# Kernel tuning notes

Measured on AMD Instinct MI355X. Metric: run time of the kernel, lower is better.

## Reference

```python
import jax, jax.numpy as jnp
import numpy as np

B, Q, D = 4, 1024, 1024
N, DH = 16, 64  # n_head, d_head
SCALE = 1.0 / DH ** 0.5
LN_EPS = 1e-5


def setup_inputs() -> dict:
    key = jax.random.key(0)
    ks = jax.random.split(key, 10)
    return {
        "w": jax.random.normal(ks[0], (B, Q, D), jnp.float32),
        "r_emb": jax.random.normal(ks[1], (Q, N, DH), jnp.float32),
        "r_w_bias": jax.random.normal(ks[2], (N, DH), jnp.float32),
        "r_bias": jax.random.normal(ks[3], (Q, N), jnp.float32),
        # projection weights stored [in, out]; torch Linear init std = 1/sqrt(d_head)
        "Wq": jax.random.normal(ks[4], (D, N * DH), jnp.float32) * SCALE,
        "Wk": jax.random.normal(ks[5], (D, N * DH), jnp.float32) * SCALE,
        "Wv": jax.random.normal(ks[6], (D, N * DH), jnp.float32) * SCALE,
        "Wo": jax.random.normal(ks[7], (N * DH, D), jnp.float32) * SCALE,
        "ln_gamma": jnp.ones((D,), jnp.float32),
        "ln_beta": jnp.zeros((D,), jnp.float32),
    }


def _rel_shift(x):
    # x: [b, i, j, n]; pad a zero column at the end of j then drop j=0
    # equivalent to shifting left by one along j with a trailing zero.
    return jnp.concatenate([x[:, :, 1:, :], jnp.zeros_like(x[:, :, :1, :])], axis=2)


def reference(w, r_emb, r_w_bias, r_bias, Wq, Wk, Wv, Wo, ln_gamma, ln_beta):
    b, qlen, d = w.shape
    klen = qlen  # mems=None
    n, dh = r_w_bias.shape

    q_h = (w @ Wq).reshape(b, qlen, n, dh)
    k_h = (w @ Wk).reshape(b, klen, n, dh)
    v_h = (w @ Wv).reshape(b, klen, n, dh)

    rw_q = q_h + r_w_bias[None, None]                      # [b,q,n,dh]
    AC = jnp.einsum('bind,bjnd->bijn', rw_q, k_h)          # [b,q,k,n]
    B_ = jnp.einsum('bind,jnd->bijn', q_h, r_emb)          # [b,q,k,n]
    BD = _rel_shift(B_ + r_bias[None, None])               # [b,q,k,n]

    attn_score = (AC + BD) * SCALE
    attn_prob = jax.nn.softmax(attn_score, axis=2)
    attn_vec = jnp.einsum('bijn,bjnd->bind', attn_prob, v_h)
    attn_out = attn_vec.reshape(b, qlen, n * dh) @ Wo

    out = w + attn_out  # residual (post-lnorm path)
    mu = jnp.mean(out, axis=-1, keepdims=True)
    var = jnp.var(out, axis=-1, keepdims=True)
    return (out - mu) / jnp.sqrt(var + LN_EPS) * ln_gamma + ln_beta
```

## Files before the change

### kernel.cpp

```cpp
#include <hip/hip_runtime.h>
#include <hip/hip_bf16.h>

using f16 = _Float16;
typedef _Float16 f16x8 __attribute__((ext_vector_type(8)));
typedef _Float16 f16x4 __attribute__((ext_vector_type(4)));
typedef float f32x4 __attribute__((ext_vector_type(4)));

#define AS1 __attribute__((address_space(1)))
#define AS3 __attribute__((address_space(3)))

constexpr int Bc = 4, Qc = 1024, Dc = 1024, Nh = 16, DHc = 64;
constexpr int BQ = Bc * Qc;
constexpr int NHEAD = Bc * Nh;
constexpr float ATT_SCALE = 0.125f;
constexpr float LOG2E = 1.44269504088896f;

struct Ptr4 { const float* p[4]; };
__global__ __launch_bounds__(256) void k_prep(
    const float* __restrict__ w_in, f16* __restrict__ wh,
    Ptr4 srcs, f16* __restrict__ WT,
    const float* __restrict__ remb, f16* __restrict__ Ke)
{
    const int bid = blockIdx.x, tid = threadIdx.x;
    if (bid < 2048) {
        long i8 = ((long)bid * 256 + tid) * 8;
        float4 a = *(const float4*)&w_in[i8];
        float4 b = *(const float4*)&w_in[i8 + 4];
        f16x8 o = { (f16)a.x, (f16)a.y, (f16)a.z, (f16)a.w,
                    (f16)b.x, (f16)b.y, (f16)b.z, (f16)b.w };
        *(f16x8*)&wh[i8] = o;
    } else if (bid < 6144) {
        __shared__ f16 tile[32][33];
        int idx = bid - 2048;
        int z = idx >> 10, rem = idx & 1023;
        int r0 = (rem >> 5) * 32, c0 = (rem & 31) * 32;
        const float* src = srcs.p[z];
        f16* d = WT + (long)z * Dc * Dc;
        int tx = tid & 31, ty = tid >> 5;
#pragma unroll
        for (int dy = 0; dy < 32; dy += 8) {
            int r = r0 + ty + dy, c = c0 + tx;
            tile[ty + dy][tx] = (f16)src[(long)r * Dc + c];
        }
        __syncthreads();
#pragma unroll
        for (int dy = 0; dy < 32; dy += 8) {
            int c = c0 + ty + dy, r = r0 + tx;
            d[(long)c * Dc + r] = tile[tx][ty + dy];
        }
    } else {
        long gid = (long)(bid - 6144) * 256 + tid;
        int d8 = (int)(gid & 7) * 8;
        int j = (int)((gid >> 3) & 1023);
        int h = (int)(gid >> 13);
        int n = h & 15;
        f16x8 kv;
        if (j < 1023) {
            const float* rp = &remb[((long)(j + 1) * 16 + n) * 64 + d8];
            float4 r0 = *(const float4*)rp, r1 = *(const float4*)(rp + 4);
            kv[0] = (f16)r0.x; kv[1] = (f16)r0.y; kv[2] = (f16)r0.z; kv[3] = (f16)r0.w;
            kv[4] = (f16)r1.x; kv[5] = (f16)r1.y; kv[6] = (f16)r1.z; kv[7] = (f16)r1.w;
        } else {
            kv = f16x8{};
        }
        *(f16x8*)&Ke[(((long)h << 10) + j) * 64 + d8] = kv;
    }
}

__global__ __launch_bounds__(256) void k_fold(
    f16* __restrict__ kh, const f16* __restrict__ Ke,
    const float* __restrict__ rwb, const float* __restrict__ rbias,
    float* __restrict__ ckrb)
{
    long gid = (long)blockIdx.x * 256 + threadIdx.x;
    int t8 = (int)(gid & 7);
    long seg = gid >> 3;
    int n = (int)(seg & 15);
    long gm = seg >> 4;
    int b = (int)(gm >> 10), j = (int)(gm & 1023);

    f16* kp = &kh[gm * 1024 + n * 64 + t8 * 8];
    f16x8 kv = *(f16x8*)kp;
    f16x8 ke = *(const f16x8*)&Ke[(((long)(b * 16 + n) << 10) + j) * 64 + t8 * 8];

    float dot = 0.0f;
    f16x8 ko;
#pragma unroll
    for (int e = 0; e < 8; ++e) {
        float kf = (float)kv[e];
        dot += kf * rwb[n * 64 + t8 * 8 + e];
        ko[e] = (f16)(kf + (float)ke[e]);
    }
    *(f16x8*)kp = ko;

    dot += __shfl_xor(dot, 1);
    dot += __shfl_xor(dot, 2);
    dot += __shfl_xor(dot, 4);
    if (t8 == 0) {
        float rbv = (j < 1023) ? rbias[(j + 1) * 16 + n] : 0.0f;
        ckrb[(((long)(b * 16 + n)) << 10) + j] = (dot + rbv) * (ATT_SCALE * LOG2E);
    }
}

template <int BM, int BN, int BK, int WROWS, int WCOLS, int EPI>
__global__ __launch_bounds__(256) void k_gemm_nt(
    const f16* __restrict__ A, const f16* __restrict__ Bt, void* __restrict__ Cv,
    f16* __restrict__ qtp, f16* __restrict__ ktp, f16* __restrict__ vtp,
    int lda, int ldb, int ldc, int K)
{
    static_assert(BK == 64, "geometry below assumes BK=64");
    constexpr int TM = BM / (WROWS * 16);
    constexpr int TN = BN / (WCOLS * 16);
    __shared__ __align__(16) f16 sA[BM * 64];
    __shared__ __align__(16) f16 sB[BN * 64];

    const int tid = threadIdx.x;
    const int lane = tid & 63, wave = tid >> 6;
    const int wm = wave / WCOLS, wn = wave % WCOLS;

    const int nwg = gridDim.x * gridDim.y;
    const int flat = blockIdx.y * gridDim.x + blockIdx.x;
    const int cpx = nwg >> 3;
    const int swz = (flat & 7) * cpx + (flat >> 3);
    const int bx = swz % gridDim.x, by = swz / gridDim.x;
    const int m0 = by * BM, n0 = bx * BN;

    f32x4 acc[TM][TN] = {};

    const int lrow = lane & 15;
    const int quad = lane >> 4;
    const int srow = lane >> 3;
    const int scol = ((lane & 7) ^ (srow & 7)) * 8;

    for (int k0 = 0; k0 < K; k0 += 64) {
        __syncthreads();
        constexpr int CHA = BM / 8;
#pragma unroll
        for (int ch = 0; ch < CHA / 4; ++ch) {
            int cc = ch * 4 + wave;
            __builtin_amdgcn_global_load_lds(
                (const AS1 void*)(const void*)&A[(long)(m0 + cc * 8 + srow) * lda + k0 + scol],
                (AS3 void*)(void*)&sA[cc * 512], 16, 0, 0);
        }
        constexpr int CHB = BN / 8;
#pragma unroll
        for (int ch = 0; ch < CHB / 4; ++ch) {
            int cc = ch * 4 + wave;
            __builtin_amdgcn_global_load_lds(
                (const AS1 void*)(const void*)&Bt[(long)(n0 + cc * 8 + srow) * ldb + k0 + scol],
                (AS3 void*)(void*)&sB[cc * 512], 16, 0, 0);
        }
        __syncthreads();

#pragma unroll
        for (int kk = 0; kk < 2; ++kk) {
            const int kcb = kk * 4 + quad;
            f16x8 af[TM], bfr[TN];
#pragma unroll
            for (int mi = 0; mi < TM; ++mi) {
                int R = wm * TM * 16 + mi * 16 + lrow;
                af[mi] = *(const f16x8*)&sA[R * 64 + ((kcb ^ (lrow & 7)) * 8)];
            }
#pragma unroll
            for (int ni = 0; ni < TN; ++ni) {
                int R = wn * TN * 16 + ni * 16 + lrow;
                bfr[ni] = *(const f16x8*)&sB[R * 64 + ((kcb ^ (lrow & 7)) * 8)];
            }
#pragma unroll
            for (int mi = 0; mi < TM; ++mi)
#pragma unroll
                for (int ni = 0; ni < TN; ++ni)
                    acc[mi][ni] = __builtin_amdgcn_mfma_f32_16x16x32_f16(af[mi], bfr[ni], acc[mi][ni], 0, 0, 0);
        }
    }

    const int crow = (lane >> 4) * 4;
    const int ccol = lane & 15;
#pragma unroll
    for (int mi = 0; mi < TM; ++mi)
#pragma unroll
        for (int ni = 0; ni < TN; ++ni)
#pragma unroll
            for (int r = 0; r < 4; ++r) {
                int gm = m0 + wm * TM * 16 + mi * 16 + crow + r;
                int gn = n0 + wn * TN * 16 + ni * 16 + ccol;
                float val = acc[mi][ni][r];
                if constexpr (EPI == 0) {
                    ((f16*)Cv)[(long)gm * ldc + gn] = (f16)val;
                } else {
                    int seg = n0 >> 10;
                    int col = gn & 1023;
                    if (seg == 0) {
                        qtp[(long)gm * 1024 + col] = (f16)val;
                    } else if (seg == 1) {
                        ktp[(long)gm * 1024 + col] = (f16)val;
                    } else {
                        int b = gm >> 10, i = gm & 1023;
                        vtp[(((long)(b << 10) + col) << 10) + i] = (f16)val;
                    }
                }
            }
}

__global__ __launch_bounds__(512, 4) void k_flash(
    const f16* __restrict__ qh, const f16* __restrict__ kh,
    const f16* __restrict__ vT, const float* __restrict__ ckrb,
    f16* __restrict__ avp)
{
    __shared__ __align__(16) f16 sKa[2][128 * 64];
    __shared__ __align__(16) f16 sVa[2][64 * 128];
    __shared__ float sRB[2][128];

    const int tid = threadIdx.x, lane = tid & 63, wave = tid >> 6;
    const int bid = blockIdx.x;
    const int h = (((bid >> 3) & 7) << 3) | (bid & 7);
    const int i0 = (bid >> 6) * 128;
    const int b = h >> 4, n = h & 15;

    const int lrow = lane & 15;
    const int quad = lane >> 4;

    const int lr3 = lane >> 3;
    const int swcK = (lane & 7) ^ (lr3 & 7);
    const f16* srcK = kh + ((long)(b * Qc) + 16 * wave + lr3) * 1024 + n * 64 + swcK * 8;

    const int lv4 = lane >> 4;
    const int c16 = lane & 15;
    const int d0 = 8 * wave + lv4;
    const int swcV0 = (c16 & 8) | ((c16 & 7) ^ (d0 & 7));
    const int swcV1 = (c16 & 8) | ((c16 & 7) ^ ((d0 + 4) & 7));
    const f16* srcVb = vT + (long)h * DHc * Qc;

    const f16 qsc = (f16)0.125f;
    f16x8 aq[2];
    {
        long rix = (long)(b * Qc + i0 + wave * 16 + lrow) * 1024 + n * 64;
        aq[0] = *(const f16x8*)&qh[rix + quad * 8] * qsc;
        aq[1] = *(const f16x8*)&qh[rix + 32 + quad * 8] * qsc;
    }

    auto stage = [&](int buf, int j0) {
        __builtin_amdgcn_global_load_lds((const AS1 void*)(srcK + (long)j0 * 1024),
                                         (AS3 void*)&sKa[buf][wave * 1024], 16, 0, 0);
        __builtin_amdgcn_global_load_lds((const AS1 void*)(srcK + (long)(j0 + 8) * 1024),
                                         (AS3 void*)&sKa[buf][wave * 1024 + 512], 16, 0, 0);
        __builtin_amdgcn_global_load_lds((const AS1 void*)(srcVb + (long)d0 * Qc + j0 + swcV0 * 8),
                                         (AS3 void*)&sVa[buf][wave * 1024], 16, 0, 0);
        __builtin_amdgcn_global_load_lds((const AS1 void*)(srcVb + (long)(d0 + 4) * Qc + j0 + swcV1 * 8),
                                         (AS3 void*)&sVa[buf][wave * 1024 + 512], 16, 0, 0);
    };

    float m_i = -1e30f, l_i = 0.0f;
    f32x4 o_acc[4] = {};

    {
        float rbv = 0.0f;
        if (tid < 128) rbv = ckrb[((long)h << 10) + tid];
        stage(0, 0);
        if (tid < 128) sRB[0][tid] = rbv;
    }
    __syncthreads();

    for (int jt = 0; jt < 8; ++jt) {
        const int cur = jt & 1;

        float rbn = 0.0f;
        if (jt < 7) {
            const int j0n = (jt + 1) * 128;
            stage(cur ^ 1, j0n);
            if (tid < 128) rbn = ckrb[((long)h << 10) + j0n + tid];
        }

        const f16* Ka = &sKa[cur][0];
        const f16* Va = &sVa[cur][0];
        const int rsw = lrow & 7;

        f32x4 s_acc[8] = {};
#pragma unroll
        for (int ni = 0; ni < 8; ++ni) {
            int rb_ = (ni * 16 + lrow) * 64;
            f16x8 a0 = *(const f16x8*)&Ka[rb_ + ((0 + quad) ^ rsw) * 8];
            f16x8 a1 = *(const f16x8*)&Ka[rb_ + ((4 + quad) ^ rsw) * 8];
            s_acc[ni] = __builtin_amdgcn_mfma_f32_16x16x32_f16(a0, aq[0], s_acc[ni], 0, 0, 0);
            s_acc[ni] = __builtin_amdgcn_mfma_f32_16x16x32_f16(a1, aq[1], s_acc[ni], 0, 0, 0);
        }

        f16x4 pf[8];
        float mx = -1e30f, sm = 0.0f;
#pragma unroll
        for (int ni = 0; ni < 8; ++ni) {
            f32x4 rb4 = *(const f32x4*)&sRB[cur][ni * 16 + quad * 4];
            f16x4 pvv;
#pragma unroll
            for (int r = 0; r < 4; ++r) {
                float v = fmaf(s_acc[ni][r], LOG2E, rb4[r]);
                s_acc[ni][r] = v;
                mx = fmaxf(mx, v);
                float e = __builtin_amdgcn_exp2f(v - m_i);
                sm += e;
                pvv[r] = (f16)e;
            }
            pf[ni] = pvv;
        }
        if (!__all(mx - m_i <= 8.0f)) {
            float wmx = fmaxf(mx, __shfl_xor(mx, 16));
            wmx = fmaxf(wmx, __shfl_xor(wmx, 32));
            float mn = fmaxf(m_i, wmx);
            float alpha = __builtin_amdgcn_exp2f(m_i - mn);
            sm = 0.0f;
#pragma unroll
            for (int ni = 0; ni < 8; ++ni) {
                f16x4 pvv;
#pragma unroll
                for (int r = 0; r < 4; ++r) {
                    float e = __builtin_amdgcn_exp2f(s_acc[ni][r] - mn);
                    sm += e;
                    pvv[r] = (f16)e;
                }
                pf[ni] = pvv;
            }
            l_i *= alpha;
#pragma unroll
            for (int r = 0; r < 4; ++r) {
                float al = __shfl(alpha, quad * 4 + r);
#pragma unroll
                for (int dt = 0; dt < 4; ++dt) o_acc[dt][r] *= al;
            }
            m_i = mn;
        }
        l_i += sm;

#pragma unroll
        for (int nj = 0; nj < 8; ++nj) {
            int c = 2 * nj + (quad >> 1);
            int coff = ((c & 8) | ((c & 7) ^ rsw)) * 8 + (quad & 1) * 4;
#pragma unroll
            for (int dt = 0; dt < 4; ++dt) {
                f16x4 bv = *(const f16x4*)&Va[(dt * 16 + lrow) * 128 + coff];
                o_acc[dt] = __builtin_amdgcn_mfma_f32_16x16x16f16(pf[nj], bv, o_acc[dt], 0, 0, 0);
            }
        }

        if (jt < 7) {
            if (tid < 128) sRB[cur ^ 1][tid] = rbn;
            __syncthreads();
        }
    }

    l_i += __shfl_xor(l_i, 16);
    l_i += __shfl_xor(l_i, 32);
    {
        float linv = 1.0f / l_i;
#pragma unroll
        for (int r = 0; r < 4; ++r) {
            float li = __shfl(linv, quad * 4 + r);
            int i = i0 + wave * 16 + quad * 4 + r;
#pragma unroll
            for (int dt = 0; dt < 4; ++dt) {
                int d = dt * 16 + lrow;
                avp[((long)(b * Qc + i) << 10) + n * 64 + d] = (f16)(o_acc[dt][r] * li);
            }
        }
    }
}

__global__ __launch_bounds__(256) void k_res_ln(const float* __restrict__ w, const f16* __restrict__ ao,
                                                const float* __restrict__ gamma, const float* __restrict__ beta,
                                                float* __restrict__ out) {
    const long base = (long)blockIdx.x * 1024;
    const int tid = threadIdx.x;
    float4 wv = *(const float4*)&w[base + tid * 4];
    f16x4 av = *(const f16x4*)&ao[base + tid * 4];
    float x[4] = { wv.x + (float)av[0], wv.y + (float)av[1],
                   wv.z + (float)av[2], wv.w + (float)av[3] };
    float s = x[0] + x[1] + x[2] + x[3];
    float s2 = x[0] * x[0] + x[1] * x[1] + x[2] * x[2] + x[3] * x[3];
#pragma unroll
    for (int off = 32; off; off >>= 1) { s += __shfl_down(s, off); s2 += __shfl_down(s2, off); }
    __shared__ float rs[4], rs2[4];
    if ((tid & 63) == 0) { rs[tid >> 6] = s; rs2[tid >> 6] = s2; }
    __syncthreads();
    s = rs[0] + rs[1] + rs[2] + rs[3];
    s2 = rs2[0] + rs2[1] + rs2[2] + rs2[3];
    float mu = s * (1.0f / 1024.0f);
    float var = s2 * (1.0f / 1024.0f) - mu * mu;
    float inv = rsqrtf(var + 1e-5f);
    float4 gv = *(const float4*)&gamma[tid * 4];
    float4 bv = *(const float4*)&beta[tid * 4];
    float4 o;
    o.x = (x[0] - mu) * inv * gv.x + bv.x;
    o.y = (x[1] - mu) * inv * gv.y + bv.y;
    o.z = (x[2] - mu) * inv * gv.z + bv.z;
    o.w = (x[3] - mu) * inv * gv.w + bv.w;
    *(float4*)&out[base + tid * 4] = o;
}

extern "C" void kernel_launch(void* const* d_in, const int* in_sizes, int n_in,
                              void* d_out, int out_size, void* d_ws, size_t ws_size,
                              hipStream_t stream) {
    const float* w_in   = (const float*)d_in[0];
    const float* r_emb  = (const float*)d_in[1];
    const float* r_wb   = (const float*)d_in[2];
    const float* r_bias = (const float*)d_in[3];
    const float* Wq     = (const float*)d_in[4];
    const float* Wk     = (const float*)d_in[5];
    const float* Wv     = (const float*)d_in[6];
    const float* Wo     = (const float*)d_in[7];
    const float* ln_g   = (const float*)d_in[8];
    const float* ln_b   = (const float*)d_in[9];
    float* out = (float*)d_out;

    char* p = (char*)d_ws;
    auto alloc = [&](size_t bytes) { char* r = p; p += (bytes + 255) & ~(size_t)255; return r; };
    f16* wh = (f16*)alloc((size_t)BQ * Dc * 2);
    f16* WT = (f16*)alloc((size_t)4 * Dc * Dc * 2);
    f16* qh = (f16*)alloc((size_t)BQ * Dc * 2);
    f16* kh = (f16*)alloc((size_t)BQ * Dc * 2);
    f16* Ke = (f16*)alloc((size_t)NHEAD * Qc * DHc * 2);
    f16* vT = (f16*)alloc((size_t)BQ * Dc * 2);
    float* ckrb = (float*)alloc((size_t)NHEAD * Qc * 4);
    f16* WoT = WT + (size_t)3 * Dc * Dc;
    f16* avp = wh;
    f16* ao  = Ke;

    Ptr4 srcs{{Wq, Wk, Wv, Wo}};
    k_prep<<<8192, 256, 0, stream>>>(w_in, wh, srcs, WT, r_emb, Ke);

    k_gemm_nt<128, 128, 64, 2, 2, 5><<<dim3(3 * Dc / 128, BQ / 128), 256, 0, stream>>>(
        wh, WT, nullptr, qh, kh, vT, Dc, Dc, 0, Dc);

    k_fold<<<2048, 256, 0, stream>>>(kh, Ke, r_wb, r_bias, ckrb);

    k_flash<<<512, 512, 0, stream>>>(qh, kh, vT, ckrb, avp);

    k_gemm_nt<64, 128, 64, 2, 2, 0><<<dim3(Dc / 128, BQ / 64), 256, 0, stream>>>(
        avp, WoT, ao, nullptr, nullptr, nullptr, Dc, Dc, Dc, Dc);

    k_res_ln<<<BQ, 256, 0, stream>>>(w_in, ao, ln_g, ln_b, out);
}
```

Before: 200.4 us.

## Triple-buffer GEMM LDS staging with BK=32 and async prefetch two tiles ahead

Restructures the NT GEMM main loop from a single-buffered BK=64 tile, with two barriers per iteration, into a three-stage ring of BK=32 LDS buffers. Direct global-to-LDS loads for tile kt+2 are issued before computing tile kt, and explicit vmcnt waits plus one barrier per step replace the old sync pattern. This is meant to hide global load latency behind MFMA work in both the QKV and output projections. In exchange there are more loop iterations with fewer MFMAs each, a new LDS swizzle for 32-wide rows, and manual vmcnt counting that must match the number of issued loads.

Result: slower. 205.4 us (+2.5%).

```diff
diff --git a/kernel.cpp b/kernel.cpp
--- a/kernel.cpp
+++ b/kernel.cpp
@@ -102,17 +102,17 @@
     }
 }
 
-template <int BM, int BN, int BK, int WROWS, int WCOLS, int EPI>
+template <int BM, int BN, int WROWS, int WCOLS, int EPI>
 __global__ __launch_bounds__(256) void k_gemm_nt(
     const f16* __restrict__ A, const f16* __restrict__ Bt, void* __restrict__ Cv,
     f16* __restrict__ qtp, f16* __restrict__ ktp, f16* __restrict__ vtp,
     int lda, int ldb, int ldc, int K)
 {
-    static_assert(BK == 64, "geometry below assumes BK=64");
     constexpr int TM = BM / (WROWS * 16);
     constexpr int TN = BN / (WCOLS * 16);
-    __shared__ __align__(16) f16 sA[BM * 64];
-    __shared__ __align__(16) f16 sB[BN * 64];
+    constexpr int LPS = BM / 64 + BN / 64;
+    __shared__ __align__(16) f16 sA[3][BM * 32];
+    __shared__ __align__(16) f16 sB[3][BN * 32];
 
     const int tid = threadIdx.x;
     const int lane = tid & 63, wave = tid >> 6;
@@ -129,48 +129,61 @@
 
     const int lrow = lane & 15;
     const int quad = lane >> 4;
-    const int srow = lane >> 3;
-    const int scol = ((lane & 7) ^ (srow & 7)) * 8;
-
-    for (int k0 = 0; k0 < K; k0 += 64) {
-        __syncthreads();
-        constexpr int CHA = BM / 8;
+    const int srow = lane >> 2;
+    const int scol = ((lane & 3) ^ ((srow >> 1) & 3)) * 8;
+    const int rsw2 = (lrow >> 1) & 3;
+
+    auto stage = [&](int buf, int kt) {
+        const int k0 = kt * 32;
+        constexpr int CHA = BM / 16;
 #pragma unroll
         for (int ch = 0; ch < CHA / 4; ++ch) {
             int cc = ch * 4 + wave;
             __builtin_amdgcn_global_load_lds(
-                (const AS1 void*)(const void*)&A[(long)(m0 + cc * 8 + srow) * lda + k0 + scol],
-                (AS3 void*)(void*)&sA[cc * 512], 16, 0, 0);
-        }
-        constexpr int CHB = BN / 8;
+                (const AS1 void*)(const void*)&A[(long)(m0 + cc * 16 + srow) * lda + k0 + scol],
+                (AS3 void*)(void*)&sA[buf][cc * 512], 16, 0, 0);
+        }
+        constexpr int CHB = BN / 16;
 #pragma unroll
         for (int ch = 0; ch < CHB / 4; ++ch) {
             int cc = ch * 4 + wave;
             __builtin_amdgcn_global_load_lds(
-                (const AS1 void*)(const void*)&Bt[(long)(n0 + cc * 8 + srow) * ldb + k0 + scol],
-                (AS3 void*)(void*)&sB[cc * 512], 16, 0, 0);
-        }
-        __syncthreads();
-
-#pragma unroll
-        for (int kk = 0; kk < 2; ++kk) {
-            const int kcb = kk * 4 + quad;
-            f16x8 af[TM], bfr[TN];
-#pragma unroll
-            for (int mi = 0; mi < TM; ++mi) {
-                int R = wm * TM * 16 + mi * 16 + lrow;
-                af[mi] = *(const f16x8*)&sA[R * 64 + ((kcb ^ (lrow & 7)) * 8)];
-            }
-#pragma unroll
-            for (int ni = 0; ni < TN; ++ni) {
-                int R = wn * TN * 16 + ni * 16 + lrow;
-                bfr[ni] = *(const f16x8*)&sB[R * 64 + ((kcb ^ (lrow & 7)) * 8)];
-            }
-#pragma unroll
-            for (int mi = 0; mi < TM; ++mi)
-#pragma unroll
-                for (int ni = 0; ni < TN; ++ni)
-                    acc[mi][ni] = __builtin_amdgcn_mfma_f32_16x16x32_f16(af[mi], bfr[ni], acc[mi][ni], 0, 0, 0);
+                (const AS1 void*)(const void*)&Bt[(long)(n0 + cc * 16 + srow) * ldb + k0 + scol],
+                (AS3 void*)(void*)&sB[buf][cc * 512], 16, 0, 0);
+        }
+    };
+
+    const int NKT = K / 32;
+    stage(0, 0);
+    stage(1, 1);
+    asm volatile("s_waitcnt vmcnt(%0)" :: "i"(LPS) : "memory");
+    __builtin_amdgcn_s_barrier();
+
+    for (int kt = 0; kt < NKT; ++kt) {
+        const int cur = kt % 3;
+        if (kt + 2 < NKT) stage((kt + 2) % 3, kt + 2);
+
+        f16x8 af[TM], bfr[TN];
+#pragma unroll
+        for (int mi = 0; mi < TM; ++mi) {
+            int R = wm * TM * 16 + mi * 16 + lrow;
+            af[mi] = *(const f16x8*)&sA[cur][R * 32 + (quad ^ rsw2) * 8];
+        }
+#pragma unroll
+        for (int ni = 0; ni < TN; ++ni) {
+            int R = wn * TN * 16 + ni * 16 + lrow;
+            bfr[ni] = *(const f16x8*)&sB[cur][R * 32 + (quad ^ rsw2) * 8];
+        }
+#pragma unroll
+        for (int mi = 0; mi < TM; ++mi)
+#pragma unroll
+            for (int ni = 0; ni < TN; ++ni)
+                acc[mi][ni] = __builtin_amdgcn_mfma_f32_16x16x32_f16(af[mi], bfr[ni], acc[mi][ni], 0, 0, 0);
+
+        if (kt + 1 < NKT) {
+            if (kt + 2 < NKT) asm volatile("s_waitcnt vmcnt(%0)" :: "i"(LPS) : "memory");
+            else              asm volatile("s_waitcnt vmcnt(0)" ::: "memory");
+            __builtin_amdgcn_s_barrier();
         }
     }
 
@@ -426,14 +439,14 @@
     Ptr4 srcs{{Wq, Wk, Wv, Wo}};
     k_prep<<<8192, 256, 0, stream>>>(w_in, wh, srcs, WT, r_emb, Ke);
 
-    k_gemm_nt<128, 128, 64, 2, 2, 5><<<dim3(3 * Dc / 128, BQ / 128), 256, 0, stream>>>(
+    k_gemm_nt<128, 128, 2, 2, 5><<<dim3(3 * Dc / 128, BQ / 128), 256, 0, stream>>>(
         wh, WT, nullptr, qh, kh, vT, Dc, Dc, 0, Dc);
 
     k_fold<<<2048, 256, 0, stream>>>(kh, Ke, r_wb, r_bias, ckrb);
 
     k_flash<<<512, 512, 0, stream>>>(qh, kh, vT, ckrb, avp);
 
-    k_gemm_nt<64, 128, 64, 2, 2, 0><<<dim3(Dc / 128, BQ / 64), 256, 0, stream>>>(
+    k_gemm_nt<64, 128, 2, 2, 0><<<dim3(Dc / 128, BQ / 64), 256, 0, stream>>>(
         avp, WoT, ao, nullptr, nullptr, nullptr, Dc, Dc, Dc, Dc);
 
     k_res_ln<<<BQ, 256, 0, stream>>>(w_in, ao, ln_g, ln_b, out);
```
